# Kernel tuning notes

Hardware: AMD Instinct MI355X
Metric: run time of the kernel (lower is better)

Reference implementation:

```python
import jax, jax.numpy as jnp
import numpy as np

B, S, HID, HEADS, INTER = 64, 512, 40, 4, 20
DH = HID // HEADS  # 10
EPS = 1e-5


def layer_norm(x, g, b):
    mu = jnp.mean(x, axis=-1, keepdims=True)
    var = jnp.mean(jnp.square(x - mu), axis=-1, keepdims=True)
    return (x - mu) * jax.lax.rsqrt(var + EPS) * g + b


def setup_inputs() -> dict:
    key = jax.random.key(0)
    ks = jax.random.split(key, 16)
    s = 0.05
    return {
        "hidden_states": jax.random.normal(ks[0], (B, S, HID), jnp.float32),
        "ln1_g": jnp.ones((HID,), jnp.float32),
        "ln1_b": jnp.zeros((HID,), jnp.float32),
        "Wq": jax.random.normal(ks[1], (HID, HID), jnp.float32) * s,
        "bq": jnp.zeros((HID,), jnp.float32),
        "Wk": jax.random.normal(ks[2], (HID, HID), jnp.float32) * s,
        "bk": jnp.zeros((HID,), jnp.float32),
        "Wv": jax.random.normal(ks[3], (HID, HID), jnp.float32) * s,
        "bv": jnp.zeros((HID,), jnp.float32),
        "Wo": jax.random.normal(ks[4], (HID, HID), jnp.float32) * s,
        "bo": jnp.zeros((HID,), jnp.float32),
        "ln2_g": jnp.ones((HID,), jnp.float32),
        "ln2_b": jnp.zeros((HID,), jnp.float32),
        "W1": jax.random.normal(ks[5], (HID, INTER), jnp.float32) * s,
        "b1": jnp.zeros((INTER,), jnp.float32),
        "W2": jax.random.normal(ks[6], (INTER, HID), jnp.float32) * s,
        "b2": jnp.zeros((HID,), jnp.float32),
    }


def reference(hidden_states, ln1_g, ln1_b, Wq, bq, Wk, bk, Wv, bv, Wo, bo,
              ln2_g, ln2_b, W1, b1, W2, b2):
    x = hidden_states
    # --- self-attention (pre-LN) ---
    h = layer_norm(x, ln1_g, ln1_b)
    q = (h @ Wq + bq).reshape(B, S, HEADS, DH)
    k = (h @ Wk + bk).reshape(B, S, HEADS, DH)
    v = (h @ Wv + bv).reshape(B, S, HEADS, DH)
    # scores: [B, H, S, S]
    scores = jnp.einsum('bqhd,bkhd->bhqk', q, k) / jnp.sqrt(jnp.float32(DH))
    probs = jax.nn.softmax(scores, axis=-1)
    ctx = jnp.einsum('bhqk,bkhd->bqhd', probs, v).reshape(B, S, HID)
    attn_out = ctx @ Wo + bo + x
    # --- FFN (pre-LN) ---
    h2 = layer_norm(attn_out, ln2_g, ln2_b)
    inter = jax.nn.gelu(h2 @ W1 + b1, approximate=False)
    out = inter @ W2 + b2 + attn_out
    return out
```

## Files before the change

### kernel.cpp

```cpp
#include <hip/hip_runtime.h>
#include <stdint.h>

#define BB 64
#define SS 512
#define EPSF 1e-5f

typedef __attribute__((ext_vector_type(8)))  short bh8;
typedef __attribute__((ext_vector_type(16))) float fx16;
typedef __attribute__((ext_vector_type(4)))  int   i32x4;

__device__ __forceinline__ int cvtpk(float a, float b) {
    int r;
    asm("v_cvt_pk_bf16_f32 %0, %1, %2" : "=v"(r) : "v"(a), "v"(b));
    return r;
}

__global__ __launch_bounds__(256) void k_ln_qkv(
    const float* __restrict__ x, const float* __restrict__ g, const float* __restrict__ be,
    const float* __restrict__ Wq, const float* __restrict__ bq,
    const float* __restrict__ Wk, const float* __restrict__ bk,
    const float* __restrict__ Wv, const float* __restrict__ bv,
    unsigned short* __restrict__ qo, unsigned short* __restrict__ ko,
    unsigned short* __restrict__ vt)
{
    __shared__ float sX[64][41];

    const int tid = threadIdx.x;
    const float4* xblk = (const float4*)(x + (size_t)blockIdx.x * 64 * 40);
    for (int idx = tid; idx < 640; idx += 256) {
        float4 u = xblk[idx];
        int fl = idx * 4;
        int r = fl / 40, c = fl - r * 40;
        sX[r][c] = u.x; sX[r][c + 1] = u.y; sX[r][c + 2] = u.z; sX[r][c + 3] = u.w;
    }
    __syncthreads();

    const int lane = tid & 63;
    const int part = tid >> 6;
    const int hp = __builtin_amdgcn_readfirstlane(part);

    float s1 = 0.f, s2 = 0.f;
#pragma unroll 8
    for (int i = 0; i < 40; i++) { float v = sX[lane][i]; s1 += v; s2 += v * v; }
    const float mu = s1 * 0.025f;
    const float rs = rsqrtf(s2 * 0.025f - mu * mu + EPSF);

    float hrow[40];
#pragma unroll 4
    for (int i = 0; i < 40; i++)
        hrow[i] = (sX[lane][i] - mu) * rs * g[i] + be[i];

    const float* Wp[3] = {Wq, Wk, Wv};
    const float* Bp[3] = {bq, bk, bv};

    float acc[3][10];
#pragma unroll
    for (int w = 0; w < 3; w++)
#pragma unroll
        for (int c = 0; c < 10; c++) acc[w][c] = Bp[w][hp * 10 + c];

#pragma unroll 2
    for (int i = 0; i < 40; i++) {
        const float hi = hrow[i];
#pragma unroll
        for (int w = 0; w < 3; w++) {
            const float* wp = Wp[w] + i * 40 + hp * 10;
#pragma unroll
            for (int c = 0; c < 10; c++) acc[w][c] += hi * wp[c];
        }
    }

    const float cs = 1.4426950408889634f / 3.1622776601683795f;
#pragma unroll
    for (int c = 0; c < 10; c++) acc[0][c] *= cs;

    const int row0 = blockIdx.x * 64;
    const int b4 = (row0 >> 9) * 4, s0 = row0 & 511;
    const size_t srow = (size_t)(b4 + hp) * 512 + s0 + lane;

    {
        int p0 = cvtpk(acc[0][0], acc[0][1]);
        int p1 = cvtpk(acc[0][2], acc[0][3]);
        int p2 = cvtpk(acc[0][4], acc[0][5]);
        int p3 = cvtpk(acc[0][6], acc[0][7]);
        int p4 = cvtpk(acc[0][8], acc[0][9]);
        i32x4* dst = (i32x4*)qo + srow * 2;
        dst[0] = (i32x4){p0, p1, p2, p3};
        dst[1] = (i32x4){p4, 0, 0, 0};
    }
    {
        int p0 = cvtpk(acc[1][0], acc[1][1]);
        int p1 = cvtpk(acc[1][2], acc[1][3]);
        int p2 = cvtpk(acc[1][4], acc[1][5]);
        int p3 = cvtpk(acc[1][6], acc[1][7]);
        int p4 = cvtpk(acc[1][8], acc[1][9]);
        i32x4* dst = (i32x4*)ko + srow * 2;
        dst[0] = (i32x4){p0, p1, p2, p3};
        dst[1] = (i32x4){p4, 0, 0, 0};
    }
    {
        int p0 = cvtpk(acc[2][0], acc[2][1]);
        int p1 = cvtpk(acc[2][2], acc[2][3]);
        int p2 = cvtpk(acc[2][4], acc[2][5]);
        int p3 = cvtpk(acc[2][6], acc[2][7]);
        int p4 = cvtpk(acc[2][8], acc[2][9]);
        unsigned short* vb = vt + ((size_t)(b4 + hp) * 16) * 512 + (s0 + lane);
        vb[0 * 512] = (unsigned short)(p0 & 0xffff);
        vb[1 * 512] = (unsigned short)((unsigned)p0 >> 16);
        vb[2 * 512] = (unsigned short)(p1 & 0xffff);
        vb[3 * 512] = (unsigned short)((unsigned)p1 >> 16);
        vb[4 * 512] = (unsigned short)(p2 & 0xffff);
        vb[5 * 512] = (unsigned short)((unsigned)p2 >> 16);
        vb[6 * 512] = (unsigned short)(p3 & 0xffff);
        vb[7 * 512] = (unsigned short)((unsigned)p3 >> 16);
        vb[8 * 512] = (unsigned short)(p4 & 0xffff);
        vb[9 * 512] = (unsigned short)((unsigned)p4 >> 16);
        vb[10 * 512] = 0x3F80;
        vb[11 * 512] = 0; vb[12 * 512] = 0; vb[13 * 512] = 0;
        vb[14 * 512] = 0; vb[15 * 512] = 0;
    }
}

__global__ __launch_bounds__(256) void k_attn(
    const unsigned short* __restrict__ qg, const unsigned short* __restrict__ kg,
    const unsigned short* __restrict__ vt, float* __restrict__ ctx)
{
    __shared__ __align__(16) char smem[24576 + 16640];

    const int tid = threadIdx.x;
    const int bh = blockIdx.x >> 1;
    const int qh = blockIdx.x & 1;
    const int lane = tid & 63;
    const int wave = tid >> 6;

    bh8 qf0, qf1;
    {
        const char* qp = (const char*)qg + (size_t)bh * 512 * 32;
        const int qbase = qh * 256 + wave * 64;
        qf0 = *(const bh8*)(qp + (size_t)(qbase + (lane & 31)) * 32 + (lane >> 5) * 16);
        qf1 = *(const bh8*)(qp + (size_t)(qbase + 32 + (lane & 31)) * 32 + (lane >> 5) * 16);
    }
    {
        const i32x4* gk = (const i32x4*)((const char*)kg + (size_t)bh * 512 * 32);
        for (int c = tid; c < 1024; c += 256) {
            i32x4 u = gk[c];
            *(i32x4*)(smem + (c >> 1) * 48 + (c & 1) * 16) = u;
        }
        const i32x4* gv = (const i32x4*)((const char*)vt + (size_t)bh * 16 * 1024);
        for (int c = tid; c < 1024; c += 256) {
            i32x4 u = gv[c];
            *(i32x4*)(smem + 24576 + (c >> 6) * 1040 + (c & 63) * 16) = u;
        }
    }
    __syncthreads();

    const char* sK = smem;
    const char* sV = smem + 24576;
    const int krow = lane & 31, khalf = lane >> 5;
    const int vrow = lane & 15;
    const bool vzero = (lane & 16) != 0;

    fx16 acc0 = (fx16)(0.0f), acc1 = (fx16)(0.0f);

    for (int kt = 0; kt < 16; ++kt) {
        bh8 kf  = *(const bh8*)(sK + (kt * 32 + krow) * 48 + khalf * 16);
        bh8 vf0 = *(const bh8*)(sV + vrow * 1040 + kt * 64 + khalf * 16);
        bh8 vf1 = *(const bh8*)(sV + vrow * 1040 + kt * 64 + 32 + khalf * 16);
        if (vzero) { vf0 = (bh8)(short)0; vf1 = (bh8)(short)0; }
#pragma unroll
        for (int qt = 0; qt < 2; ++qt) {
            fx16 s = __builtin_amdgcn_mfma_f32_32x32x16_bf16(
                kf, qt ? qf1 : qf0, (fx16)(0.0f), 0, 0, 0);
            float e[16];
#pragma unroll
            for (int r = 0; r < 16; ++r) e[r] = __builtin_amdgcn_exp2f(s[r]);
            int c0 = cvtpk(e[0], e[1]),   c1 = cvtpk(e[2], e[3]);
            int c2 = cvtpk(e[4], e[5]),   c3 = cvtpk(e[6], e[7]);
            int c4 = cvtpk(e[8], e[9]),   c5 = cvtpk(e[10], e[11]);
            int c6 = cvtpk(e[12], e[13]), c7 = cvtpk(e[14], e[15]);
            asm("v_permlane32_swap_b32 %0, %1" : "+v"(c0), "+v"(c2));
            asm("v_permlane32_swap_b32 %0, %1" : "+v"(c1), "+v"(c3));
            asm("v_permlane32_swap_b32 %0, %1" : "+v"(c4), "+v"(c6));
            asm("v_permlane32_swap_b32 %0, %1" : "+v"(c5), "+v"(c7));
            union { i32x4 i; bh8 h; } lo, hi;
            lo.i = (i32x4){c0, c1, c2, c3};
            hi.i = (i32x4){c4, c5, c6, c7};
            if (qt == 0) {
                acc0 = __builtin_amdgcn_mfma_f32_32x32x16_bf16(lo.h, vf0, acc0, 0, 0, 0);
                acc0 = __builtin_amdgcn_mfma_f32_32x32x16_bf16(hi.h, vf1, acc0, 0, 0, 0);
            } else {
                acc1 = __builtin_amdgcn_mfma_f32_32x32x16_bf16(lo.h, vf0, acc1, 0, 0, 0);
                acc1 = __builtin_amdgcn_mfma_f32_32x32x16_bf16(hi.h, vf1, acc1, 0, 0, 0);
            }
        }
    }

    const int d = lane & 31;
    const int qb = qh * 256 + wave * 64;
#pragma unroll
    for (int qt = 0; qt < 2; ++qt) {
        fx16 A = qt ? acc1 : acc0;
#pragma unroll
        for (int r = 0; r < 16; ++r) {
            float v = A[r];
            float ls = __shfl(v, (lane & 32) | 10, 64);
            float o = v / ls;
            if (d < 10) {
                int q = qb + qt * 32 + (r & 3) + 8 * (r >> 2) + 4 * (lane >> 5);
                ctx[((size_t)bh * 512 + q) * 10 + d] = o;
            }
        }
    }
}

__global__ __launch_bounds__(256) void k_out_ffn(
    const float* __restrict__ ctx, const float* __restrict__ x,
    const float* __restrict__ Wo, const float* __restrict__ bo,
    const float* __restrict__ g2, const float* __restrict__ bt2,
    const float* __restrict__ W1, const float* __restrict__ b1,
    const float* __restrict__ W2, const float* __restrict__ b2,
    float* __restrict__ out)
{
    __shared__ float sWo[40][48];
    __shared__ float sW1[40][32];
    __shared__ float sW2[20][48];
    __shared__ float sBo[40], sG2[40], sBt2[40], sB1[20], sB2[40];
    __shared__ float sCtx[64][41];
    __shared__ float sH[64][41];
    __shared__ float sIt[64][21];
    __shared__ float sSum[64][4], sSum2[64][4];

    const int tid = threadIdx.x;
    for (int idx = tid; idx < 1600; idx += 256) {
        int i = idx / 40, j = idx % 40;
        sWo[i][(j / 10) * 12 + (j % 10)] = Wo[idx];
    }
    for (int idx = tid; idx < 800; idx += 256) {
        {
            int i = idx / 20, j = idx % 20;
            sW1[i][(j / 5) * 8 + (j % 5)] = W1[idx];
        }
        {
            int i = idx / 40, j = idx % 40;
            sW2[i][(j / 10) * 12 + (j % 10)] = W2[idx];
        }
    }
    if (tid < 40) { sBo[tid] = bo[tid]; sG2[tid] = g2[tid]; sBt2[tid] = bt2[tid]; sB2[tid] = b2[tid]; }
    if (tid < 20) sB1[tid] = b1[tid];

    const int row0 = blockIdx.x * 64;
    const int b = row0 >> 9, s0 = row0 & 511;

    for (int idx = tid; idx < 640; idx += 256) {
        const int hh = idx / 160, f = idx - hh * 160;
        float4 u = *(const float4*)(ctx + ((size_t)((b * 4 + hh) * 512 + s0)) * 10 + f * 4);
        const int fo = f * 4;
        float e[4] = {u.x, u.y, u.z, u.w};
#pragma unroll
        for (int t = 0; t < 4; t++) {
            const int fe = fo + t;
            const int r = fe / 10, c = fe - r * 10;
            sCtx[r][hh * 10 + c] = e[t];
        }
    }
    const float4* xblk = (const float4*)(x + (size_t)blockIdx.x * 64 * 40);
    for (int idx = tid; idx < 640; idx += 256) {
        float4 w = xblk[idx];
        int fl = idx * 4;
        int r = fl / 40, c = fl - r * 40;
        sH[r][c] = w.x; sH[r][c + 1] = w.y; sH[r][c + 2] = w.z; sH[r][c + 3] = w.w;
    }
    __syncthreads();

    const int lane = tid & 63;
    const int wv = tid >> 6;
    const int j0 = wv * 10;

    float acc[10];
#pragma unroll
    for (int j = 0; j < 10; j++) acc[j] = sBo[j0 + j] + sH[lane][j0 + j];
#pragma unroll 8
    for (int i = 0; i < 40; i++) {
        const float ci = sCtx[lane][i];
        const float4* wrow = (const float4*)&sWo[i][wv * 12];
        float4 w0 = wrow[0], w1 = wrow[1], w2 = wrow[2];
        acc[0] += ci * w0.x; acc[1] += ci * w0.y; acc[2] += ci * w0.z; acc[3] += ci * w0.w;
        acc[4] += ci * w1.x; acc[5] += ci * w1.y; acc[6] += ci * w1.z; acc[7] += ci * w1.w;
        acc[8] += ci * w2.x; acc[9] += ci * w2.y;
    }
    {
        float s1 = 0.f, s2 = 0.f;
#pragma unroll
        for (int j = 0; j < 10; j++) { s1 += acc[j]; s2 += acc[j] * acc[j]; }
        sSum[lane][wv] = s1; sSum2[lane][wv] = s2;
    }
    __syncthreads();
    const float mu = (sSum[lane][0] + sSum[lane][1] + sSum[lane][2] + sSum[lane][3]) * 0.025f;
    const float ex2 = (sSum2[lane][0] + sSum2[lane][1] + sSum2[lane][2] + sSum2[lane][3]) * 0.025f;
    const float rs = rsqrtf(ex2 - mu * mu + EPSF);
#pragma unroll
    for (int j = 0; j < 10; j++)
        sH[lane][j0 + j] = (acc[j] - mu) * rs * sG2[j0 + j] + sBt2[j0 + j];
    __syncthreads();

    const int f0 = wv * 5;
    float it[5];
#pragma unroll
    for (int j = 0; j < 5; j++) it[j] = sB1[f0 + j];
#pragma unroll 8
    for (int i = 0; i < 40; i++) {
        const float hi = sH[lane][i];
        const float4* wrow = (const float4*)&sW1[i][wv * 8];
        float4 w0 = wrow[0], w1 = wrow[1];
        it[0] += hi * w0.x; it[1] += hi * w0.y; it[2] += hi * w0.z; it[3] += hi * w0.w;
        it[4] += hi * w1.x;
    }
#pragma unroll
    for (int j = 0; j < 5; j++) {
        float t = it[j];
        sIt[lane][f0 + j] = 0.5f * t * (1.0f + erff(t * 0.70710678118654752f));
    }
    __syncthreads();

    float o[10];
#pragma unroll
    for (int j = 0; j < 10; j++) o[j] = acc[j] + sB2[j0 + j];
#pragma unroll 4
    for (int i = 0; i < 20; i++) {
        const float ii = sIt[lane][i];
        const float4* wrow = (const float4*)&sW2[i][wv * 12];
        float4 w0 = wrow[0], w1 = wrow[1], w2 = wrow[2];
        o[0] += ii * w0.x; o[1] += ii * w0.y; o[2] += ii * w0.z; o[3] += ii * w0.w;
        o[4] += ii * w1.x; o[5] += ii * w1.y; o[6] += ii * w1.z; o[7] += ii * w1.w;
        o[8] += ii * w2.x; o[9] += ii * w2.y;
    }
#pragma unroll
    for (int j = 0; j < 10; j++) sCtx[lane][j0 + j] = o[j];
    __syncthreads();

    float4* oblk = (float4*)(out + (size_t)blockIdx.x * 64 * 40);
    for (int idx = tid; idx < 640; idx += 256) {
        int fl = idx * 4;
        int r = fl / 40, c = fl - r * 40;
        float4 u;
        u.x = sCtx[r][c]; u.y = sCtx[r][c + 1]; u.z = sCtx[r][c + 2]; u.w = sCtx[r][c + 3];
        oblk[idx] = u;
    }
}

extern "C" void kernel_launch(void* const* d_in, const int* in_sizes, int n_in,
                              void* d_out, int out_size, void* d_ws, size_t ws_size,
                              hipStream_t stream)
{
    const float* x   = (const float*)d_in[0];
    const float* g1  = (const float*)d_in[1];
    const float* be1 = (const float*)d_in[2];
    const float* Wq  = (const float*)d_in[3];
    const float* bq  = (const float*)d_in[4];
    const float* Wk  = (const float*)d_in[5];
    const float* bk  = (const float*)d_in[6];
    const float* Wv  = (const float*)d_in[7];
    const float* bv  = (const float*)d_in[8];
    const float* Wo  = (const float*)d_in[9];
    const float* bo  = (const float*)d_in[10];
    const float* g2  = (const float*)d_in[11];
    const float* bt2 = (const float*)d_in[12];
    const float* W1  = (const float*)d_in[13];
    const float* b1  = (const float*)d_in[14];
    const float* W2  = (const float*)d_in[15];
    const float* b2  = (const float*)d_in[16];

    unsigned short* wsu = (unsigned short*)d_ws;
    const size_t T = (size_t)256 * 512 * 16;
    unsigned short* q  = wsu;
    unsigned short* k  = wsu + T;
    unsigned short* vt = wsu + 2 * T;
    float* ctx = (float*)(wsu + 3 * T);

    k_ln_qkv<<<512, 256, 0, stream>>>(x, g1, be1, Wq, bq, Wk, bk, Wv, bv, q, k, vt);
    k_attn<<<512, 256, 0, stream>>>(q, k, vt, ctx);
    k_out_ffn<<<512, 256, 0, stream>>>(ctx, x, Wo, bo, g2, bt2, W1, b1, W2, b2,
                                       (float*)d_out);
}
```

Baseline: 140.1 us.

## Fuse three kernels into one cooperative kernel with grid syncs

Merges the LN+QKV, attention, and out-proj+FFN kernels into one cooperative kernel of 512 blocks, separated by grid-wide syncs. Shared memory is reused across phases through a union-like buffer. This removes two kernel launch gaps and their tails. In exchange, every block must be co-resident (launch_bounds 256,2), and each grid barrier costs time and forces all blocks to wait for the slowest one.

```diff
diff --git a/kernel.cpp b/kernel.cpp
--- a/kernel.cpp
+++ b/kernel.cpp
@@ -1,8 +1,9 @@
 #include <hip/hip_runtime.h>
+#include <hip/hip_cooperative_groups.h>
 #include <stdint.h>
 
-#define BB 64
-#define SS 512
+namespace cg = cooperative_groups;
+
 #define EPSF 1e-5f
 
 typedef __attribute__((ext_vector_type(8)))  short bh8;
@@ -15,336 +16,334 @@
     return r;
 }
 
-__global__ __launch_bounds__(256) void k_ln_qkv(
-    const float* __restrict__ x, const float* __restrict__ g, const float* __restrict__ be,
-    const float* __restrict__ Wq, const float* __restrict__ bq,
-    const float* __restrict__ Wk, const float* __restrict__ bk,
-    const float* __restrict__ Wv, const float* __restrict__ bv,
-    unsigned short* __restrict__ qo, unsigned short* __restrict__ ko,
-    unsigned short* __restrict__ vt)
+struct P3S {
+    float sWo[40][48];
+    float sW1[40][32];
+    float sW2[20][48];
+    float sBo[40], sG2[40], sBt2[40], sB1[20], sB2[40];
+    float sCtx[64][41];
+    float sH[64][41];
+    float sIt[64][21];
+    float sSum[64][4], sSum2[64][4];
+};
+
+struct Params {
+    const float *x, *g1, *be1, *Wq, *bq, *Wk, *bk, *Wv, *bv;
+    const float *Wo, *bo, *g2, *bt2, *W1, *b1, *W2, *b2;
+    unsigned short *q, *k, *vt;
+    float *ctx, *out;
+};
+
+__global__ __launch_bounds__(256, 2) void kmega(Params P)
 {
-    __shared__ float sX[64][41];
-
-    const int tid = threadIdx.x;
-    const float4* xblk = (const float4*)(x + (size_t)blockIdx.x * 64 * 40);
-    for (int idx = tid; idx < 640; idx += 256) {
-        float4 u = xblk[idx];
-        int fl = idx * 4;
-        int r = fl / 40, c = fl - r * 40;
-        sX[r][c] = u.x; sX[r][c + 1] = u.y; sX[r][c + 2] = u.z; sX[r][c + 3] = u.w;
+    __shared__ __align__(16) char smem[sizeof(P3S)];
+
+    const int tid  = threadIdx.x;
+    const int blk  = blockIdx.x;
+    const int lane = tid & 63;
+    const int wavei = tid >> 6;
+
+    {
+        float (*sX)[41] = (float (*)[41])smem;
+        const float4* xblk = (const float4*)(P.x + (size_t)blk * 64 * 40);
+        for (int idx = tid; idx < 640; idx += 256) {
+            float4 u = xblk[idx];
+            int fl = idx * 4;
+            int r = fl / 40, c = fl - r * 40;
+            sX[r][c] = u.x; sX[r][c + 1] = u.y; sX[r][c + 2] = u.z; sX[r][c + 3] = u.w;
+        }
+        __syncthreads();
+
+        const int hp = __builtin_amdgcn_readfirstlane(wavei);
+
+        float s1 = 0.f, s2 = 0.f;
+#pragma unroll 8
+        for (int i = 0; i < 40; i++) { float v = sX[lane][i]; s1 += v; s2 += v * v; }
+        const float mu = s1 * 0.025f;
+        const float rs = rsqrtf(s2 * 0.025f - mu * mu + EPSF);
+
+        float hrow[40];
+#pragma unroll 4
+        for (int i = 0; i < 40; i++)
+            hrow[i] = (sX[lane][i] - mu) * rs * P.g1[i] + P.be1[i];
+
+        const float* Wp[3] = {P.Wq, P.Wk, P.Wv};
+        const float* Bp[3] = {P.bq, P.bk, P.bv};
+
+        float acc[3][10];
+#pragma unroll
+        for (int w = 0; w < 3; w++)
+#pragma unroll
+            for (int c = 0; c < 10; c++) acc[w][c] = Bp[w][hp * 10 + c];
+
+#pragma unroll 2
+        for (int i = 0; i < 40; i++) {
+            const float hi = hrow[i];
+#pragma unroll
+            for (int w = 0; w < 3; w++) {
+                const float* wp = Wp[w] + i * 40 + hp * 10;
+#pragma unroll
+                for (int c = 0; c < 10; c++) acc[w][c] += hi * wp[c];
+            }
+        }
+
+        const float cs = 1.4426950408889634f / 3.1622776601683795f;
+#pragma unroll
+        for (int c = 0; c < 10; c++) acc[0][c] *= cs;
+
+        const int row0 = blk * 64;
+        const int b4 = (row0 >> 9) * 4, s0 = row0 & 511;
+        const size_t srow = (size_t)(b4 + hp) * 512 + s0 + lane;
+
+        {
+            int p0 = cvtpk(acc[0][0], acc[0][1]);
+            int p1 = cvtpk(acc[0][2], acc[0][3]);
+            int p2 = cvtpk(acc[0][4], acc[0][5]);
+            int p3 = cvtpk(acc[0][6], acc[0][7]);
+            int p4 = cvtpk(acc[0][8], acc[0][9]);
+            i32x4* dst = (i32x4*)P.q + srow * 2;
+            dst[0] = (i32x4){p0, p1, p2, p3};
+            dst[1] = (i32x4){p4, 0, 0, 0};
+        }
+        {
+            int p0 = cvtpk(acc[1][0], acc[1][1]);
+            int p1 = cvtpk(acc[1][2], acc[1][3]);
+            int p2 = cvtpk(acc[1][4], acc[1][5]);
+            int p3 = cvtpk(acc[1][6], acc[1][7]);
+            int p4 = cvtpk(acc[1][8], acc[1][9]);
+            i32x4* dst = (i32x4*)P.k + srow * 2;
+            dst[0] = (i32x4){p0, p1, p2, p3};
+            dst[1] = (i32x4){p4, 0, 0, 0};
+        }
+        {
+            int p0 = cvtpk(acc[2][0], acc[2][1]);
+            int p1 = cvtpk(acc[2][2], acc[2][3]);
+            int p2 = cvtpk(acc[2][4], acc[2][5]);
+            int p3 = cvtpk(acc[2][6], acc[2][7]);
+            int p4 = cvtpk(acc[2][8], acc[2][9]);
+            unsigned short* vb = P.vt + ((size_t)(b4 + hp) * 16) * 512 + (s0 + lane);
+            vb[0 * 512] = (unsigned short)(p0 & 0xffff);
+            vb[1 * 512] = (unsigned short)((unsigned)p0 >> 16);
+            vb[2 * 512] = (unsigned short)(p1 & 0xffff);
+            vb[3 * 512] = (unsigned short)((unsigned)p1 >> 16);
+            vb[4 * 512] = (unsigned short)(p2 & 0xffff);
+            vb[5 * 512] = (unsigned short)((unsigned)p2 >> 16);
+            vb[6 * 512] = (unsigned short)(p3 & 0xffff);
+            vb[7 * 512] = (unsigned short)((unsigned)p3 >> 16);
+            vb[8 * 512] = (unsigned short)(p4 & 0xffff);
+            vb[9 * 512] = (unsigned short)((unsigned)p4 >> 16);
+            vb[10 * 512] = 0x3F80;
+            vb[11 * 512] = 0; vb[12 * 512] = 0; vb[13 * 512] = 0;
+            vb[14 * 512] = 0; vb[15 * 512] = 0;
+        }
     }
-    __syncthreads();
-
-    const int lane = tid & 63;
-    const int part = tid >> 6;
-    const int hp = __builtin_amdgcn_readfirstlane(part);
-
-    float s1 = 0.f, s2 = 0.f;
+
+    __threadfence();
+    cg::this_grid().sync();
+
+    {
+        const int bh = blk >> 1;
+        const int qh = blk & 1;
+
+        bh8 qf0, qf1;
+        {
+            const char* qp = (const char*)P.q + (size_t)bh * 512 * 32;
+            const int qbase = qh * 256 + wavei * 64;
+            qf0 = *(const bh8*)(qp + (size_t)(qbase + (lane & 31)) * 32 + (lane >> 5) * 16);
+            qf1 = *(const bh8*)(qp + (size_t)(qbase + 32 + (lane & 31)) * 32 + (lane >> 5) * 16);
+        }
+        {
+            const i32x4* gk = (const i32x4*)((const char*)P.k + (size_t)bh * 512 * 32);
+            for (int c = tid; c < 1024; c += 256) {
+                i32x4 u = gk[c];
+                *(i32x4*)(smem + (c >> 1) * 48 + (c & 1) * 16) = u;
+            }
+            const i32x4* gv = (const i32x4*)((const char*)P.vt + (size_t)bh * 16 * 1024);
+            for (int c = tid; c < 1024; c += 256) {
+                i32x4 u = gv[c];
+                *(i32x4*)(smem + 24576 + (c >> 6) * 1040 + (c & 63) * 16) = u;
+            }
+        }
+        __syncthreads();
+
+        const char* sK = smem;
+        const char* sV = smem + 24576;
+        const int krow = lane & 31, khalf = lane >> 5;
+        const int vrow = lane & 15;
+        const bool vzero = (lane & 16) != 0;
+
+        fx16 acc0 = (fx16)(0.0f), acc1 = (fx16)(0.0f);
+
+        for (int kt = 0; kt < 16; ++kt) {
+            bh8 kf  = *(const bh8*)(sK + (kt * 32 + krow) * 48 + khalf * 16);
+            bh8 vf0 = *(const bh8*)(sV + vrow * 1040 + kt * 64 + khalf * 16);
+            bh8 vf1 = *(const bh8*)(sV + vrow * 1040 + kt * 64 + 32 + khalf * 16);
+            if (vzero) { vf0 = (bh8)(short)0; vf1 = (bh8)(short)0; }
+#pragma unroll
+            for (int qt = 0; qt < 2; ++qt) {
+                fx16 s = __builtin_amdgcn_mfma_f32_32x32x16_bf16(
+                    kf, qt ? qf1 : qf0, (fx16)(0.0f), 0, 0, 0);
+                float e[16];
+#pragma unroll
+                for (int r = 0; r < 16; ++r) e[r] = __builtin_amdgcn_exp2f(s[r]);
+                int c0 = cvtpk(e[0], e[1]),   c1 = cvtpk(e[2], e[3]);
+                int c2 = cvtpk(e[4], e[5]),   c3 = cvtpk(e[6], e[7]);
+                int c4 = cvtpk(e[8], e[9]),   c5 = cvtpk(e[10], e[11]);
+                int c6 = cvtpk(e[12], e[13]), c7 = cvtpk(e[14], e[15]);
+                asm("v_permlane32_swap_b32 %0, %1" : "+v"(c0), "+v"(c2));
+                asm("v_permlane32_swap_b32 %0, %1" : "+v"(c1), "+v"(c3));
+                asm("v_permlane32_swap_b32 %0, %1" : "+v"(c4), "+v"(c6));
+                asm("v_permlane32_swap_b32 %0, %1" : "+v"(c5), "+v"(c7));
+                union { i32x4 i; bh8 h; } lo, hi;
+                lo.i = (i32x4){c0, c1, c2, c3};
+                hi.i = (i32x4){c4, c5, c6, c7};
+                if (qt == 0) {
+                    acc0 = __builtin_amdgcn_mfma_f32_32x32x16_bf16(lo.h, vf0, acc0, 0, 0, 0);
+                    acc0 = __builtin_amdgcn_mfma_f32_32x32x16_bf16(hi.h, vf1, acc0, 0, 0, 0);
+                } else {
+                    acc1 = __builtin_amdgcn_mfma_f32_32x32x16_bf16(lo.h, vf0, acc1, 0, 0, 0);
+                    acc1 = __builtin_amdgcn_mfma_f32_32x32x16_bf16(hi.h, vf1, acc1, 0, 0, 0);
+                }
+            }
+        }
+
+        const int d = lane & 31;
+        const int qb = qh * 256 + wavei * 64;
+#pragma unroll
+        for (int qt = 0; qt < 2; ++qt) {
+            fx16 A = qt ? acc1 : acc0;
+#pragma unroll
+            for (int r = 0; r < 16; ++r) {
+                float v = A[r];
+                float ls = __shfl(v, (lane & 32) | 10, 64);
+                float o = v / ls;
+                if (d < 10) {
+                    int q = qb + qt * 32 + (r & 3) + 8 * (r >> 2) + 4 * (lane >> 5);
+                    P.ctx[((size_t)bh * 512 + q) * 10 + d] = o;
+                }
+            }
+        }
+    }
+
+    __threadfence();
+    cg::this_grid().sync();
+
+    {
+        P3S& S = *(P3S*)smem;
+
+        for (int idx = tid; idx < 1600; idx += 256) {
+            int i = idx / 40, j = idx % 40;
+            S.sWo[i][(j / 10) * 12 + (j % 10)] = P.Wo[idx];
+        }
+        for (int idx = tid; idx < 800; idx += 256) {
+            {
+                int i = idx / 20, j = idx % 20;
+                S.sW1[i][(j / 5) * 8 + (j % 5)] = P.W1[idx];
+            }
+            {
+                int i = idx / 40, j = idx % 40;
+                S.sW2[i][(j / 10) * 12 + (j % 10)] = P.W2[idx];
+            }
+        }
+        if (tid < 40) { S.sBo[tid] = P.bo[tid]; S.sG2[tid] = P.g2[tid]; S.sBt2[tid] = P.bt2[tid]; S.sB2[tid] = P.b2[tid]; }
+        if (tid < 20) S.sB1[tid] = P.b1[tid];
+
+        const int row0 = blk * 64;
+        const int b = row0 >> 9, s0 = row0 & 511;
+
+        for (int idx = tid; idx < 640; idx += 256) {
+            const int hh = idx / 160, f = idx - hh * 160;
+            float4 u = *(const float4*)(P.ctx + ((size_t)((b * 4 + hh) * 512 + s0)) * 10 + f * 4);
+            const int fo = f * 4;
+            float e[4] = {u.x, u.y, u.z, u.w};
+#pragma unroll
+            for (int t = 0; t < 4; t++) {
+                const int fe = fo + t;
+                const int r = fe / 10, c = fe - r * 10;
+                S.sCtx[r][hh * 10 + c] = e[t];
+            }
+        }
+        const float4* xblk = (const float4*)(P.x + (size_t)blk * 64 * 40);
+        for (int idx = tid; idx < 640; idx += 256) {
+            float4 w = xblk[idx];
+            int fl = idx * 4;
+            int r = fl / 40, c = fl - r * 40;
+            S.sH[r][c] = w.x; S.sH[r][c + 1] = w.y; S.sH[r][c + 2] = w.z; S.sH[r][c + 3] = w.w;
+        }
+        __syncthreads();
+
+        const int j0 = wavei * 10;
+
+        float acc[10];
+#pragma unroll
+        for (int j = 0; j < 10; j++) acc[j] = S.sBo[j0 + j] + S.sH[lane][j0 + j];
 #pragma unroll 8
-    for (int i = 0; i < 40; i++) { float v = sX[lane][i]; s1 += v; s2 += v * v; }
-    const float mu = s1 * 0.025f;
-    const float rs = rsqrtf(s2 * 0.025f - mu * mu + EPSF);
-
-    float hrow[40];
+        for (int i = 0; i < 40; i++) {
+            const float ci = S.sCtx[lane][i];
+            const float4* wrow = (const float4*)&S.sWo[i][wavei * 12];
+            float4 w0 = wrow[0], w1 = wrow[1], w2 = wrow[2];
+            acc[0] += ci * w0.x; acc[1] += ci * w0.y; acc[2] += ci * w0.z; acc[3] += ci * w0.w;
+            acc[4] += ci * w1.x; acc[5] += ci * w1.y; acc[6] += ci * w1.z; acc[7] += ci * w1.w;
+            acc[8] += ci * w2.x; acc[9] += ci * w2.y;
+        }
+        {
+            float s1 = 0.f, s2 = 0.f;
+#pragma unroll
+            for (int j = 0; j < 10; j++) { s1 += acc[j]; s2 += acc[j] * acc[j]; }
+            S.sSum[lane][wavei] = s1; S.sSum2[lane][wavei] = s2;
+        }
+        __syncthreads();
+        const float mu = (S.sSum[lane][0] + S.sSum[lane][1] + S.sSum[lane][2] + S.sSum[lane][3]) * 0.025f;
+        const float ex2 = (S.sSum2[lane][0] + S.sSum2[lane][1] + S.sSum2[lane][2] + S.sSum2[lane][3]) * 0.025f;
+        const float rs = rsqrtf(ex2 - mu * mu + EPSF);
+#pragma unroll
+        for (int j = 0; j < 10; j++)
+            S.sH[lane][j0 + j] = (acc[j] - mu) * rs * S.sG2[j0 + j] + S.sBt2[j0 + j];
+        __syncthreads();
+
+        const int f0 = wavei * 5;
+        float it[5];
+#pragma unroll
+        for (int j = 0; j < 5; j++) it[j] = S.sB1[f0 + j];
+#pragma unroll 8
+        for (int i = 0; i < 40; i++) {
+            const float hi = S.sH[lane][i];
+            const float4* wrow = (const float4*)&S.sW1[i][wavei * 8];
+            float4 w0 = wrow[0], w1 = wrow[1];
+            it[0] += hi * w0.x; it[1] += hi * w0.y; it[2] += hi * w0.z; it[3] += hi * w0.w;
+            it[4] += hi * w1.x;
+        }
+#pragma unroll
+        for (int j = 0; j < 5; j++) {
+            float t = it[j];
+            S.sIt[lane][f0 + j] = 0.5f * t * (1.0f + erff(t * 0.70710678118654752f));
+        }
+        __syncthreads();
+
+        float o[10];
+#pragma unroll
+        for (int j = 0; j < 10; j++) o[j] = acc[j] + S.sB2[j0 + j];
 #pragma unroll 4
-    for (int i = 0; i < 40; i++)
-        hrow[i] = (sX[lane][i] - mu) * rs * g[i] + be[i];
-
-    const float* Wp[3] = {Wq, Wk, Wv};
-    const float* Bp[3] = {bq, bk, bv};
-
-    float acc[3][10];
-#pragma unroll
-    for (int w = 0; w < 3; w++)
-#pragma unroll
-        for (int c = 0; c < 10; c++) acc[w][c] = Bp[w][hp * 10 + c];
-
-#pragma unroll 2
-    for (int i = 0; i < 40; i++) {
-        const float hi = hrow[i];
-#pragma unroll
-        for (int w = 0; w < 3; w++) {
-            const float* wp = Wp[w] + i * 40 + hp * 10;
-#pragma unroll
-            for (int c = 0; c < 10; c++) acc[w][c] += hi * wp[c];
-        }
-    }
-
-    const float cs = 1.4426950408889634f / 3.1622776601683795f;
-#pragma unroll
-    for (int c = 0; c < 10; c++) acc[0][c] *= cs;
-
-    const int row0 = blockIdx.x * 64;
-    const int b4 = (row0 >> 9) * 4, s0 = row0 & 511;
-    const size_t srow = (size_t)(b4 + hp) * 512 + s0 + lane;
-
-    {
-        int p0 = cvtpk(acc[0][0], acc[0][1]);
-        int p1 = cvtpk(acc[0][2], acc[0][3]);
-        int p2 = cvtpk(acc[0][4], acc[0][5]);
-        int p3 = cvtpk(acc[0][6], acc[0][7]);
-        int p4 = cvtpk(acc[0][8], acc[0][9]);
-        i32x4* dst = (i32x4*)qo + srow * 2;
-        dst[0] = (i32x4){p0, p1, p2, p3};
-        dst[1] = (i32x4){p4, 0, 0, 0};
-    }
-    {
-        int p0 = cvtpk(acc[1][0], acc[1][1]);
-        int p1 = cvtpk(acc[1][2], acc[1][3]);
-        int p2 = cvtpk(acc[1][4], acc[1][5]);
-        int p3 = cvtpk(acc[1][6], acc[1][7]);
-        int p4 = cvtpk(acc[1][8], acc[1][9]);
-        i32x4* dst = (i32x4*)ko + srow * 2;
-        dst[0] = (i32x4){p0, p1, p2, p3};
-        dst[1] = (i32x4){p4, 0, 0, 0};
-    }
-    {
-        int p0 = cvtpk(acc[2][0], acc[2][1]);
-        int p1 = cvtpk(acc[2][2], acc[2][3]);
-        int p2 = cvtpk(acc[2][4], acc[2][5]);
-        int p3 = cvtpk(acc[2][6], acc[2][7]);
-        int p4 = cvtpk(acc[2][8], acc[2][9]);
-        unsigned short* vb = vt + ((size_t)(b4 + hp) * 16) * 512 + (s0 + lane);
-        vb[0 * 512] = (unsigned short)(p0 & 0xffff);
-        vb[1 * 512] = (unsigned short)((unsigned)p0 >> 16);
-        vb[2 * 512] = (unsigned short)(p1 & 0xffff);
-        vb[3 * 512] = (unsigned short)((unsigned)p1 >> 16);
-        vb[4 * 512] = (unsigned short)(p2 & 0xffff);
-        vb[5 * 512] = (unsigned short)((unsigned)p2 >> 16);
-        vb[6 * 512] = (unsigned short)(p3 & 0xffff);
-        vb[7 * 512] = (unsigned short)((unsigned)p3 >> 16);
-        vb[8 * 512] = (unsigned short)(p4 & 0xffff);
-        vb[9 * 512] = (unsigned short)((unsigned)p4 >> 16);
-        vb[10 * 512] = 0x3F80;
-        vb[11 * 512] = 0; vb[12 * 512] = 0; vb[13 * 512] = 0;
-        vb[14 * 512] = 0; vb[15 * 512] = 0;
-    }
-}
-
-__global__ __launch_bounds__(256) void k_attn(
-    const unsigned short* __restrict__ qg, const unsigned short* __restrict__ kg,
-    const unsigned short* __restrict__ vt, float* __restrict__ ctx)
-{
-    __shared__ __align__(16) char smem[24576 + 16640];
-
-    const int tid = threadIdx.x;
-    const int bh = blockIdx.x >> 1;
-    const int qh = blockIdx.x & 1;
-    const int lane = tid & 63;
-    const int wave = tid >> 6;
-
-    bh8 qf0, qf1;
-    {
-        const char* qp = (const char*)qg + (size_t)bh * 512 * 32;
-        const int qbase = qh * 256 + wave * 64;
-        qf0 = *(const bh8*)(qp + (size_t)(qbase + (lane & 31)) * 32 + (lane >> 5) * 16);
-        qf1 = *(const bh8*)(qp + (size_t)(qbase + 32 + (lane & 31)) * 32 + (lane >> 5) * 16);
-    }
-    {
-        const i32x4* gk = (const i32x4*)((const char*)kg + (size_t)bh * 512 * 32);
-        for (int c = tid; c < 1024; c += 256) {
-            i32x4 u = gk[c];
-            *(i32x4*)(smem + (c >> 1) * 48 + (c & 1) * 16) = u;
-        }
-        const i32x4* gv = (const i32x4*)((const char*)vt + (size_t)bh * 16 * 1024);
-        for (int c = tid; c < 1024; c += 256) {
-            i32x4 u = gv[c];
-            *(i32x4*)(smem + 24576 + (c >> 6) * 1040 + (c & 63) * 16) = u;
-        }
-    }
-    __syncthreads();
-
-    const char* sK = smem;
-    const char* sV = smem + 24576;
-    const int krow = lane & 31, khalf = lane >> 5;
-    const int vrow = lane & 15;
-    const bool vzero = (lane & 16) != 0;
-
-    fx16 acc0 = (fx16)(0.0f), acc1 = (fx16)(0.0f);
-
-    for (int kt = 0; kt < 16; ++kt) {
-        bh8 kf  = *(const bh8*)(sK + (kt * 32 + krow) * 48 + khalf * 16);
-        bh8 vf0 = *(const bh8*)(sV + vrow * 1040 + kt * 64 + khalf * 16);
-        bh8 vf1 = *(const bh8*)(sV + vrow * 1040 + kt * 64 + 32 + khalf * 16);
-        if (vzero) { vf0 = (bh8)(short)0; vf1 = (bh8)(short)0; }
-#pragma unroll
-        for (int qt = 0; qt < 2; ++qt) {
-            fx16 s = __builtin_amdgcn_mfma_f32_32x32x16_bf16(
-                kf, qt ? qf1 : qf0, (fx16)(0.0f), 0, 0, 0);
-            float e[16];
-#pragma unroll
-            for (int r = 0; r < 16; ++r) e[r] = __builtin_amdgcn_exp2f(s[r]);
-            int c0 = cvtpk(e[0], e[1]),   c1 = cvtpk(e[2], e[3]);
-            int c2 = cvtpk(e[4], e[5]),   c3 = cvtpk(e[6], e[7]);
-            int c4 = cvtpk(e[8], e[9]),   c5 = cvtpk(e[10], e[11]);
-            int c6 = cvtpk(e[12], e[13]), c7 = cvtpk(e[14], e[15]);
-            asm("v_permlane32_swap_b32 %0, %1" : "+v"(c0), "+v"(c2));
-            asm("v_permlane32_swap_b32 %0, %1" : "+v"(c1), "+v"(c3));
-            asm("v_permlane32_swap_b32 %0, %1" : "+v"(c4), "+v"(c6));
-            asm("v_permlane32_swap_b32 %0, %1" : "+v"(c5), "+v"(c7));
-            union { i32x4 i; bh8 h; } lo, hi;
-            lo.i = (i32x4){c0, c1, c2, c3};
-            hi.i = (i32x4){c4, c5, c6, c7};
-            if (qt == 0) {
-                acc0 = __builtin_amdgcn_mfma_f32_32x32x16_bf16(lo.h, vf0, acc0, 0, 0, 0);
-                acc0 = __builtin_amdgcn_mfma_f32_32x32x16_bf16(hi.h, vf1, acc0, 0, 0, 0);
-            } else {
-                acc1 = __builtin_amdgcn_mfma_f32_32x32x16_bf16(lo.h, vf0, acc1, 0, 0, 0);
-                acc1 = __builtin_amdgcn_mfma_f32_32x32x16_bf16(hi.h, vf1, acc1, 0, 0, 0);
-            }
-        }
-    }
-
-    const int d = lane & 31;
-    const int qb = qh * 256 + wave * 64;
-#pragma unroll
-    for (int qt = 0; qt < 2; ++qt) {
-        fx16 A = qt ? acc1 : acc0;
-#pragma unroll
-        for (int r = 0; r < 16; ++r) {
-            float v = A[r];
-            float ls = __shfl(v, (lane & 32) | 10, 64);
-            float o = v / ls;
-            if (d < 10) {
-                int q = qb + qt * 32 + (r & 3) + 8 * (r >> 2) + 4 * (lane >> 5);
-                ctx[((size_t)bh * 512 + q) * 10 + d] = o;
-            }
-        }
-    }
-}
-
-__global__ __launch_bounds__(256) void k_out_ffn(
-    const float* __restrict__ ctx, const float* __restrict__ x,
-    const float* __restrict__ Wo, const float* __restrict__ bo,
-    const float* __restrict__ g2, const float* __restrict__ bt2,
-    const float* __restrict__ W1, const float* __restrict__ b1,
-    const float* __restrict__ W2, const float* __restrict__ b2,
-    float* __restrict__ out)
-{
-    __shared__ float sWo[40][48];
-    __shared__ float sW1[40][32];
-    __shared__ float sW2[20][48];
-    __shared__ float sBo[40], sG2[40], sBt2[40], sB1[20], sB2[40];
-    __shared__ float sCtx[64][41];
-    __shared__ float sH[64][41];
-    __shared__ float sIt[64][21];
-    __shared__ float sSum[64][4], sSum2[64][4];
-
-    const int tid = threadIdx.x;
-    for (int idx = tid; idx < 1600; idx += 256) {
-        int i = idx / 40, j = idx % 40;
-        sWo[i][(j / 10) * 12 + (j % 10)] = Wo[idx];
-    }
-    for (int idx = tid; idx < 800; idx += 256) {
-        {
-            int i = idx / 20, j = idx % 20;
-            sW1[i][(j / 5) * 8 + (j % 5)] = W1[idx];
-        }
-        {
-            int i = idx / 40, j = idx % 40;
-            sW2[i][(j / 10) * 12 + (j % 10)] = W2[idx];
-        }
-    }
-    if (tid < 40) { sBo[tid] = bo[tid]; sG2[tid] = g2[tid]; sBt2[tid] = bt2[tid]; sB2[tid] = b2[tid]; }
-    if (tid < 20) sB1[tid] = b1[tid];
-
-    const int row0 = blockIdx.x * 64;
-    const int b = row0 >> 9, s0 = row0 & 511;
-
-    for (int idx = tid; idx < 640; idx += 256) {
-        const int hh = idx / 160, f = idx - hh * 160;
-        float4 u = *(const float4*)(ctx + ((size_t)((b * 4 + hh) * 512 + s0)) * 10 + f * 4);
-        const int fo = f * 4;
-        float e[4] = {u.x, u.y, u.z, u.w};
-#pragma unroll
-        for (int t = 0; t < 4; t++) {
-            const int fe = fo + t;
-            const int r = fe / 10, c = fe - r * 10;
-            sCtx[r][hh * 10 + c] = e[t];
-        }
-    }
-    const float4* xblk = (const float4*)(x + (size_t)blockIdx.x * 64 * 40);
-    for (int idx = tid; idx < 640; idx += 256) {
-        float4 w = xblk[idx];
-        int fl = idx * 4;
-        int r = fl / 40, c = fl - r * 40;
-        sH[r][c] = w.x; sH[r][c + 1] = w.y; sH[r][c + 2] = w.z; sH[r][c + 3] = w.w;
-    }
-    __syncthreads();
-
-    const int lane = tid & 63;
-    const int wv = tid >> 6;
-    const int j0 = wv * 10;
-
-    float acc[10];
-#pragma unroll
-    for (int j = 0; j < 10; j++) acc[j] = sBo[j0 + j] + sH[lane][j0 + j];
-#pragma unroll 8
-    for (int i = 0; i < 40; i++) {
-        const float ci = sCtx[lane][i];
-        const float4* wrow = (const float4*)&sWo[i][wv * 12];
-        float4 w0 = wrow[0], w1 = wrow[1], w2 = wrow[2];
-        acc[0] += ci * w0.x; acc[1] += ci * w0.y; acc[2] += ci * w0.z; acc[3] += ci * w0.w;
-        acc[4] += ci * w1.x; acc[5] += ci * w1.y; acc[6] += ci * w1.z; acc[7] += ci * w1.w;
-        acc[8] += ci * w2.x; acc[9] += ci * w2.y;
-    }
-    {
-        float s1 = 0.f, s2 = 0.f;
-#pragma unroll
-        for (int j = 0; j < 10; j++) { s1 += acc[j]; s2 += acc[j] * acc[j]; }
-        sSum[lane][wv] = s1; sSum2[lane][wv] = s2;
-    }
-    __syncthreads();
-    const float mu = (sSum[lane][0] + sSum[lane][1] + sSum[lane][2] + sSum[lane][3]) * 0.025f;
-    const float ex2 = (sSum2[lane][0] + sSum2[lane][1] + sSum2[lane][2] + sSum2[lane][3]) * 0.025f;
-    const float rs = rsqrtf(ex2 - mu * mu + EPSF);
-#pragma unroll
-    for (int j = 0; j < 10; j++)
-        sH[lane][j0 + j] = (acc[j] - mu) * rs * sG2[j0 + j] + sBt2[j0 + j];
-    __syncthreads();
-
-    const int f0 = wv * 5;
-    float it[5];
-#pragma unroll
-    for (int j = 0; j < 5; j++) it[j] = sB1[f0 + j];
-#pragma unroll 8
-    for (int i = 0; i < 40; i++) {
-        const float hi = sH[lane][i];
-        const float4* wrow = (const float4*)&sW1[i][wv * 8];
-        float4 w0 = wrow[0], w1 = wrow[1];
-        it[0] += hi * w0.x; it[1] += hi * w0.y; it[2] += hi * w0.z; it[3] += hi * w0.w;
-        it[4] += hi * w1.x;
-    }
-#pragma unroll
-    for (int j = 0; j < 5; j++) {
-        float t = it[j];
-        sIt[lane][f0 + j] = 0.5f * t * (1.0f + erff(t * 0.70710678118654752f));
-    }
-    __syncthreads();
-
-    float o[10];
-#pragma unroll
-    for (int j = 0; j < 10; j++) o[j] = acc[j] + sB2[j0 + j];
-#pragma unroll 4
-    for (int i = 0; i < 20; i++) {
-        const float ii = sIt[lane][i];
-        const float4* wrow = (const float4*)&sW2[i][wv * 12];
-        float4 w0 = wrow[0], w1 = wrow[1], w2 = wrow[2];
-        o[0] += ii * w0.x; o[1] += ii * w0.y; o[2] += ii * w0.z; o[3] += ii * w0.w;
-        o[4] += ii * w1.x; o[5] += ii * w1.y; o[6] += ii * w1.z; o[7] += ii * w1.w;
-        o[8] += ii * w2.x; o[9] += ii * w2.y;
-    }
-#pragma unroll
-    for (int j = 0; j < 10; j++) sCtx[lane][j0 + j] = o[j];
-    __syncthreads();
-
-    float4* oblk = (float4*)(out + (size_t)blockIdx.x * 64 * 40);
-    for (int idx = tid; idx < 640; idx += 256) {
-        int fl = idx * 4;
-        int r = fl / 40, c = fl - r * 40;
-        float4 u;
-        u.x = sCtx[r][c]; u.y = sCtx[r][c + 1]; u.z = sCtx[r][c + 2]; u.w = sCtx[r][c + 3];
-        oblk[idx] = u;
+        for (int i = 0; i < 20; i++) {
+            const float ii = S.sIt[lane][i];
+            const float4* wrow = (const float4*)&S.sW2[i][wavei * 12];
+            float4 w0 = wrow[0], w1 = wrow[1], w2 = wrow[2];
+            o[0] += ii * w0.x; o[1] += ii * w0.y; o[2] += ii * w0.z; o[3] += ii * w0.w;
+            o[4] += ii * w1.x; o[5] += ii * w1.y; o[6] += ii * w1.z; o[7] += ii * w1.w;
+            o[8] += ii * w2.x; o[9] += ii * w2.y;
+        }
+#pragma unroll
+        for (int j = 0; j < 10; j++) S.sCtx[lane][j0 + j] = o[j];
+        __syncthreads();
+
+        float4* oblk = (float4*)(P.out + (size_t)blk * 64 * 40);
+        for (int idx = tid; idx < 640; idx += 256) {
+            int fl = idx * 4;
+            int r = fl / 40, c = fl - r * 40;
+            float4 u;
+            u.x = S.sCtx[r][c]; u.y = S.sCtx[r][c + 1]; u.z = S.sCtx[r][c + 2]; u.w = S.sCtx[r][c + 3];
+            oblk[idx] = u;
+        }
     }
 }
 
@@ -352,33 +351,33 @@
                               void* d_out, int out_size, void* d_ws, size_t ws_size,
                               hipStream_t stream)
 {
-    const float* x   = (const float*)d_in[0];
-    const float* g1  = (const float*)d_in[1];
-    const float* be1 = (const float*)d_in[2];
-    const float* Wq  = (const float*)d_in[3];
-    const float* bq  = (const float*)d_in[4];
-    const float* Wk  = (const float*)d_in[5];
-    const float* bk  = (const float*)d_in[6];
-    const float* Wv  = (const float*)d_in[7];
-    const float* bv  = (const float*)d_in[8];
-    const float* Wo  = (const float*)d_in[9];
-    const float* bo  = (const float*)d_in[10];
-    const float* g2  = (const float*)d_in[11];
-    const float* bt2 = (const float*)d_in[12];
-    const float* W1  = (const float*)d_in[13];
-    const float* b1  = (const float*)d_in[14];
-    const float* W2  = (const float*)d_in[15];
-    const float* b2  = (const float*)d_in[16];
-
     unsigned short* wsu = (unsigned short*)d_ws;
     const size_t T = (size_t)256 * 512 * 16;
-    unsigned short* q  = wsu;
-    unsigned short* k  = wsu + T;
-    unsigned short* vt = wsu + 2 * T;
-    float* ctx = (float*)(wsu + 3 * T);
-
-    k_ln_qkv<<<512, 256, 0, stream>>>(x, g1, be1, Wq, bq, Wk, bk, Wv, bv, q, k, vt);
-    k_attn<<<512, 256, 0, stream>>>(q, k, vt, ctx);
-    k_out_ffn<<<512, 256, 0, stream>>>(ctx, x, Wo, bo, g2, bt2, W1, b1, W2, b2,
-                                       (float*)d_out);
+
+    Params p;
+    p.x   = (const float*)d_in[0];
+    p.g1  = (const float*)d_in[1];
+    p.be1 = (const float*)d_in[2];
+    p.Wq  = (const float*)d_in[3];
+    p.bq  = (const float*)d_in[4];
+    p.Wk  = (const float*)d_in[5];
+    p.bk  = (const float*)d_in[6];
+    p.Wv  = (const float*)d_in[7];
+    p.bv  = (const float*)d_in[8];
+    p.Wo  = (const float*)d_in[9];
+    p.bo  = (const float*)d_in[10];
+    p.g2  = (const float*)d_in[11];
+    p.bt2 = (const float*)d_in[12];
+    p.W1  = (const float*)d_in[13];
+    p.b1  = (const float*)d_in[14];
+    p.W2  = (const float*)d_in[15];
+    p.b2  = (const float*)d_in[16];
+    p.q   = wsu;
+    p.k   = wsu + T;
+    p.vt  = wsu + 2 * T;
+    p.ctx = (float*)(wsu + 3 * T);
+    p.out = (float*)d_out;
+
+    void* args[] = { &p };
+    hipLaunchCooperativeKernel((void*)kmega, dim3(512), dim3(256), args, 0, stream);
 }
```

Measured after the change: 369.0 us. +163.3%, slower.

## Use one 512-thread block per head, stream K from global, use rcp

Applied to the files above, without the earlier changes.

The attention kernel now launches one 512-thread block per (batch, head) instead of two 256-thread blocks, so each head's K/V data is loaded once. K is no longer staged in shared memory. Each wave reads its K fragments straight from global memory and prefetches the next tile one iteration ahead. Only V stays in LDS, which cuts LDS use and may raise occupancy. The final normalisation replaces division with a hardware reciprocal, which is slightly less precise. The risk is global-load latency in the inner loop and fewer blocks in flight.

```diff
diff --git a/kernel.cpp b/kernel.cpp
--- a/kernel.cpp
+++ b/kernel.cpp
@@ -1,8 +1,6 @@
 #include <hip/hip_runtime.h>
 #include <stdint.h>
 
-#define BB 64
-#define SS 512
 #define EPSF 1e-5f
 
 typedef __attribute__((ext_vector_type(8)))  short bh8;
@@ -12,6 +10,11 @@
 __device__ __forceinline__ int cvtpk(float a, float b) {
     int r;
     asm("v_cvt_pk_bf16_f32 %0, %1, %2" : "=v"(r) : "v"(a), "v"(b));
+    return r;
+}
+__device__ __forceinline__ float fastrcp(float x) {
+    float r;
+    asm("v_rcp_f32 %0, %1" : "=v"(r) : "v"(x));
     return r;
 }
 
@@ -121,49 +124,46 @@
     }
 }
 
-__global__ __launch_bounds__(256) void k_attn(
+__global__ __launch_bounds__(512) void k_attn(
     const unsigned short* __restrict__ qg, const unsigned short* __restrict__ kg,
     const unsigned short* __restrict__ vt, float* __restrict__ ctx)
 {
-    __shared__ __align__(16) char smem[24576 + 16640];
+    __shared__ __align__(16) char smem[16640];
 
     const int tid = threadIdx.x;
-    const int bh = blockIdx.x >> 1;
-    const int qh = blockIdx.x & 1;
+    const int bh = blockIdx.x;
     const int lane = tid & 63;
-    const int wave = tid >> 6;
+    const int wavei = tid >> 6;
 
     bh8 qf0, qf1;
     {
         const char* qp = (const char*)qg + (size_t)bh * 512 * 32;
-        const int qbase = qh * 256 + wave * 64;
+        const int qbase = wavei * 64;
         qf0 = *(const bh8*)(qp + (size_t)(qbase + (lane & 31)) * 32 + (lane >> 5) * 16);
         qf1 = *(const bh8*)(qp + (size_t)(qbase + 32 + (lane & 31)) * 32 + (lane >> 5) * 16);
     }
     {
-        const i32x4* gk = (const i32x4*)((const char*)kg + (size_t)bh * 512 * 32);
-        for (int c = tid; c < 1024; c += 256) {
-            i32x4 u = gk[c];
-            *(i32x4*)(smem + (c >> 1) * 48 + (c & 1) * 16) = u;
-        }
         const i32x4* gv = (const i32x4*)((const char*)vt + (size_t)bh * 16 * 1024);
-        for (int c = tid; c < 1024; c += 256) {
+        for (int c = tid; c < 1024; c += 512) {
             i32x4 u = gv[c];
-            *(i32x4*)(smem + 24576 + (c >> 6) * 1040 + (c & 63) * 16) = u;
-        }
-    }
-    __syncthreads();
-
-    const char* sK = smem;
-    const char* sV = smem + 24576;
+            *(i32x4*)(smem + (c >> 6) * 1040 + (c & 63) * 16) = u;
+        }
+    }
+    __syncthreads();
+
+    const char* sV = smem;
     const int krow = lane & 31, khalf = lane >> 5;
     const int vrow = lane & 15;
     const bool vzero = (lane & 16) != 0;
 
+    const bh8* gk = (const bh8*)((const char*)kg + (size_t)bh * 512 * 32);
+
     fx16 acc0 = (fx16)(0.0f), acc1 = (fx16)(0.0f);
 
+    bh8 kf = gk[(size_t)krow * 2 + khalf];
     for (int kt = 0; kt < 16; ++kt) {
-        bh8 kf  = *(const bh8*)(sK + (kt * 32 + krow) * 48 + khalf * 16);
+        bh8 kfn = kf;
+        if (kt < 15) kfn = gk[(size_t)((kt + 1) * 32 + krow) * 2 + khalf];
         bh8 vf0 = *(const bh8*)(sV + vrow * 1040 + kt * 64 + khalf * 16);
         bh8 vf1 = *(const bh8*)(sV + vrow * 1040 + kt * 64 + 32 + khalf * 16);
         if (vzero) { vf0 = (bh8)(short)0; vf1 = (bh8)(short)0; }
@@ -193,10 +193,11 @@
                 acc1 = __builtin_amdgcn_mfma_f32_32x32x16_bf16(hi.h, vf1, acc1, 0, 0, 0);
             }
         }
+        kf = kfn;
     }
 
     const int d = lane & 31;
-    const int qb = qh * 256 + wave * 64;
+    const int qb = wavei * 64;
 #pragma unroll
     for (int qt = 0; qt < 2; ++qt) {
         fx16 A = qt ? acc1 : acc0;
@@ -204,7 +205,7 @@
         for (int r = 0; r < 16; ++r) {
             float v = A[r];
             float ls = __shfl(v, (lane & 32) | 10, 64);
-            float o = v / ls;
+            float o = v * fastrcp(ls);
             if (d < 10) {
                 int q = qb + qt * 32 + (r & 3) + 8 * (r >> 2) + 4 * (lane >> 5);
                 ctx[((size_t)bh * 512 + q) * 10 + d] = o;
@@ -378,7 +379,7 @@
     float* ctx = (float*)(wsu + 3 * T);
 
     k_ln_qkv<<<512, 256, 0, stream>>>(x, g1, be1, Wq, bq, Wk, bk, Wv, bv, q, k, vt);
-    k_attn<<<512, 256, 0, stream>>>(q, k, vt, ctx);
+    k_attn<<<256, 512, 0, stream>>>(q, k, vt, ctx);
     k_out_ffn<<<512, 256, 0, stream>>>(ctx, x, Wo, bo, g2, bt2, W1, b1, W2, b2,
                                        (float*)d_out);
 }
```

Result: no change. 138.7 us (-1.0%).
